# Kernel tuning notes

Measured on AMD Instinct MI355X. Metric: run time of the kernel, lower is better.

The kernel has to match this reference:

```python
import jax, jax.numpy as jnp
import numpy as np
import math

B, T, D, N = 4, 1024, 768, 7  # batch, seq, d_model, n_chambers
STEP, WARMUP = 4000, 2000      # curriculum: step past warmup -> all masks ~1
INIT_SCALE = 0.01


def _curriculum_masks():
    # NautilusScheduler.get_masks: smooth sigmoid activation per chamber (static floats)
    slope = 8.0 * N / WARMUP
    return [1.0 / (1.0 + math.exp(-slope * (STEP - WARMUP * (i + 0.5) / N))) for i in range(N)]


def _layernorm(x, g, b, eps=1e-5):
    m = jnp.mean(x, axis=-1, keepdims=True)
    v = jnp.mean((x - m) ** 2, axis=-1, keepdims=True)
    return (x - m) * jax.lax.rsqrt(v + eps) * g + b


def _chamber(h, Wq, Wk, gw, gb, sp, mask_val, causal):
    # get_bias stand-in: bilinear content bias (B,T,T)
    q = h @ Wq                                   # (B,T,D)
    k = h @ Wk                                   # (B,T,D)
    bias = jnp.einsum('btd,bsd->bts', q, k) / jnp.sqrt(jnp.asarray(D, h.dtype))
    bias = jnp.where(causal[None], bias, -jnp.inf)   # causal masked_fill
    w = jnp.nan_to_num(jax.nn.softmax(bias, axis=-1))
    enrichment = jnp.einsum('bts,bsd->btd', w, h) - h
    gate = jax.nn.sigmoid(h @ gw[:, None] + gb)      # (B,T,1)
    scale = jax.nn.softplus(sp)                      # learnable positive scale
    return scale * gate * mask_val * enrichment


def setup_inputs() -> dict:
    key = jax.random.key(0)
    ks = jax.random.split(key, 8)
    x = jax.random.normal(ks[0], (B, T, D), jnp.float32)
    s = 1.0 / np.sqrt(D)
    Wq = jax.random.normal(ks[1], (N, D, D), jnp.float32) * s
    Wk = jax.random.normal(ks[2], (N, D, D), jnp.float32) * s
    gate_w = jax.random.normal(ks[3], (N, D), jnp.float32) * 0.02
    gate_b = jnp.zeros((N,), jnp.float32)
    # per-chamber softplus-inverse init: log(exp(init*(1+3*prog))-1+1e-6)
    sp = np.array([math.log(math.exp(INIT_SCALE * (1.0 + 3.0 * i / (N - 1))) - 1.0 + 1e-6)
                   for i in range(N)], dtype=np.float32)
    scale_p = jnp.asarray(sp)
    merge_W = jax.random.normal(ks[4], (D, N * D), jnp.float32) * (1.0 / np.sqrt(N * D))
    return {
        'x': x, 'Wq': Wq, 'Wk': Wk, 'gate_w': gate_w, 'gate_b': gate_b,
        'scale_p': scale_p, 'merge_W': merge_W,
        'mode_logit': jnp.float32(0.0), 'residual_gate': jnp.float32(0.1),
        'ln_pre_g': jnp.ones((D,), jnp.float32), 'ln_pre_b': jnp.zeros((D,), jnp.float32),
        'ln_post_g': jnp.ones((D,), jnp.float32), 'ln_post_b': jnp.zeros((D,), jnp.float32),
    }


def reference(x, Wq, Wk, gate_w, gate_b, scale_p, merge_W, mode_logit,
              residual_gate, ln_pre_g, ln_pre_b, ln_post_g, ln_post_b):
    masks = _curriculum_masks()
    causal = jnp.tril(jnp.ones((T, T), bool))
    h = _layernorm(x, ln_pre_g, ln_pre_b)
    mode_gate = jax.nn.sigmoid(mode_logit)
    seq = jnp.zeros_like(h)
    deltas = []
    for i in range(N):  # fixed small structural loop over chambers
        seq = seq + _chamber(h + seq, Wq[i], Wk[i], gate_w[i], gate_b[i],
                             scale_p[i], masks[i], causal)
        deltas.append(_chamber(h, Wq[i], Wk[i], gate_w[i], gate_b[i],
                               scale_p[i], masks[i], causal))
    par = jnp.concatenate(deltas, axis=-1) @ merge_W.T  # (B,T,D)
    enrichment = (1.0 - mode_gate) * seq + mode_gate * par
    enrichment = _layernorm(enrichment, ln_post_g, ln_post_b)
    return x + residual_gate * enrichment
```

## Files before the change

kernel.cpp:

```cpp
#include <hip/hip_runtime.h>
#include <math.h>

#define D_MODEL 768
#define T_SEQ   1024
#define BATCH   4
#define NCH     7
#define ROWS    4096
#define KM      (NCH * D_MODEL)

typedef unsigned short u16;
typedef __attribute__((ext_vector_type(8))) short bh8;
typedef __attribute__((ext_vector_type(4))) float f32x4;

__device__ __forceinline__ u16 f2bf(float f) {
    union { float f; unsigned u; } v; v.f = f;
    return (u16)((v.u + 0x7fffu + ((v.u >> 16) & 1u)) >> 16);
}
__device__ __forceinline__ float bf2f(u16 b) {
    union { unsigned u; float f; } v; v.u = ((unsigned)b) << 16;
    return v.f;
}
__device__ __forceinline__ float wred_sum(float v) {
    #pragma unroll
    for (int o = 32; o; o >>= 1) v += __shfl_down(v, o, 64);
    return v;
}
__device__ __forceinline__ float wred_max(float v) {
    #pragma unroll
    for (int o = 32; o; o >>= 1) v = fmaxf(v, __shfl_down(v, o, 64));
    return v;
}
__device__ __forceinline__ float chamber_mask(int i) {
    float slope = 8.0f * 7.0f / 2000.0f;
    return 1.0f / (1.0f + __expf(-slope * (4000.0f - 2000.0f * (i + 0.5f) / 7.0f)));
}

#define GLD16(g, l) __builtin_amdgcn_global_load_lds( \
    (const __attribute__((address_space(1))) void*)(g), \
    (__attribute__((address_space(3))) void*)(l), 16, 0, 0)

__device__ __forceinline__ int xcd_swizzle(int gflat, int Ntot) {
    if ((Ntot & 7) == 0) {
        int chunk = Ntot >> 3;
        gflat = (gflat & 7) * chunk + (gflat >> 3);
    }
    return gflat;
}

__device__ __forceinline__ int slot_f(int row) { return (row >> 1) & 3; }

__global__ __launch_bounds__(256)
void gemm_nt_kernel(const u16* __restrict__ A, const u16* __restrict__ B,
                    void* __restrict__ Cv,
                    int K, int lda, int ldb, int ldc,
                    long long sA1, long long sA2, long long sB1, long long sB2,
                    long long sC1, long long sC2, int zm,
                    float alpha, int mode, int causal_skip, int causal_k,
                    int kss, int klen)
{
    int gx = gridDim.x, gy = gridDim.y;
    int Ntot = gx * gy * gridDim.z;
    int gflat = xcd_swizzle(blockIdx.x + gx * (blockIdx.y + gy * blockIdx.z), Ntot);
    int bn = gflat % gx;
    int rest = gflat / gx;
    int bm = rest % gy;
    int bz = rest / gy;
    if (causal_skip && bn > bm) return;
    int bz1 = bz % zm, bz2 = bz / zm;

    const u16* Ab = A + bz1 * sA1 + bz2 * sA2 + (long long)(bm * 128) * lda;
    const u16* Bb = B + bz1 * sB1 + bz2 * sB2 + (long long)(bn * 128) * ldb;

    __shared__ u16 sm[4 * 128 * 32];
    u16* Al0 = sm;
    u16* Bl0 = sm + 128 * 32;
    u16* Al1 = sm + 2 * 128 * 32;
    u16* Bl1 = sm + 3 * 128 * 32;

    int tid  = threadIdx.x;
    int lane = tid & 63;
    int wave = tid >> 6;
    int wm = wave >> 1, wn = wave & 1;

    int k_begin = kss ? bz1 * kss : 0;
    int k_end   = klen ? (k_begin + klen) : K;
    if (causal_k) k_end = min(k_end, (bm + 1) * 128);

    f32x4 acc[4][4];
    #pragma unroll
    for (int i = 0; i < 4; i++)
        #pragma unroll
        for (int j = 0; j < 4; j++)
            acc[i][j] = (f32x4){0.f, 0.f, 0.f, 0.f};

    int srow = lane >> 2;
    int skq  = (lane & 3) * 8;
    int fm   = lane & 15;
    int fk   = (lane >> 4) * 8;

    for (int k0 = k_begin; k0 < k_end; k0 += 64) {
        __syncthreads();
        #pragma unroll
        for (int r = 0; r < 2; r++) {
            int row = r * 64 + wave * 16 + srow;
            long long ra = (long long)row * lda + k0 + skq;
            long long rb2 = (long long)row * ldb + k0 + skq;
            GLD16(Ab + ra,       Al0 + row * 32 + skq);
            GLD16(Bb + rb2,      Bl0 + row * 32 + skq);
            GLD16(Ab + ra + 32,  Al1 + row * 32 + skq);
            GLD16(Bb + rb2 + 32, Bl1 + row * 32 + skq);
        }
        __syncthreads();

        #pragma unroll
        for (int p = 0; p < 2; p++) {
            const u16* Al = p ? Al1 : Al0;
            const u16* Bl = p ? Bl1 : Bl0;
            bh8 af[4], bf[4];
            #pragma unroll
            for (int i = 0; i < 4; i++)
                af[i] = *(const bh8*)(Al + (wm * 64 + i * 16 + fm) * 32 + fk);
            #pragma unroll
            for (int j = 0; j < 4; j++)
                bf[j] = *(const bh8*)(Bl + (wn * 64 + j * 16 + fm) * 32 + fk);
            #pragma unroll
            for (int i = 0; i < 4; i++)
                #pragma unroll
                for (int j = 0; j < 4; j++)
                    acc[i][j] = __builtin_amdgcn_mfma_f32_16x16x32_bf16(af[i], bf[j], acc[i][j], 0, 0, 0);
        }
    }

    int rbase = bm * 128 + wm * 64 + (lane >> 4) * 4;
    int cbase = bn * 128 + wn * 64 + (lane & 15);
    long long zoff = bz1 * sC1 + bz2 * sC2;
    if (mode == 1) {
        u16* C = (u16*)Cv + zoff;
        #pragma unroll
        for (int i = 0; i < 4; i++)
            #pragma unroll
            for (int j = 0; j < 4; j++)
                #pragma unroll
                for (int r = 0; r < 4; r++)
                    C[(long long)(rbase + i * 16 + r) * ldc + cbase + j * 16] = f2bf(acc[i][j][r] * alpha);
    } else if (mode == 3) {
        u16* C = (u16*)Cv + zoff;
        #pragma unroll
        for (int i = 0; i < 4; i++)
            #pragma unroll
            for (int j = 0; j < 4; j++)
                #pragma unroll
                for (int r = 0; r < 4; r++) {
                    union { _Float16 h; u16 u; } cv;
                    cv.h = (_Float16)(acc[i][j][r] * alpha);
                    C[(long long)(rbase + i * 16 + r) * ldc + cbase + j * 16] = cv.u;
                }
    } else {
        float* C = (float*)Cv + zoff;
        #pragma unroll
        for (int i = 0; i < 4; i++)
            #pragma unroll
            for (int j = 0; j < 4; j++)
                #pragma unroll
                for (int r = 0; r < 4; r++)
                    C[(long long)(rbase + i * 16 + r) * ldc + cbase + j * 16] = acc[i][j][r] * alpha;
    }
}

__global__ __launch_bounds__(256)
void gemm64_nt_kernel(const u16* __restrict__ A, const u16* __restrict__ B,
                      void* __restrict__ Cv,
                      int K, int lda, int ldb, int ldc,
                      long long sA1, long long sA2, long long sB1, long long sB2,
                      long long sC1, long long sC2, int zm,
                      float alpha, int mode, int causal_skip, int causal_k,
                      int tri, int lptrev,
                      float* __restrict__ hhfp, const float* __restrict__ coefp,
                      u16* __restrict__ hbsp, u16* __restrict__ htsp,
                      const float* __restrict__ hp, u16* __restrict__ dbp)
{
    int bn, bm, bz;
    if (tri) {
        int Ntot = gridDim.x;
        int f = xcd_swizzle(blockIdx.x, Ntot);
        bz = f / tri;
        int r = f - bz * tri;
        bm = (int)((sqrtf(8.0f * (float)r + 1.0f) - 1.0f) * 0.5f);
        while ((bm + 1) * (bm + 2) / 2 <= r) bm++;
        while (bm * (bm + 1) / 2 > r) bm--;
        bn = r - bm * (bm + 1) / 2;
    } else {
        int gx = gridDim.x, gy = gridDim.y;
        int Ntot = gx * gy * gridDim.z;
        int gflat = xcd_swizzle(blockIdx.x + gx * (blockIdx.y + gy * blockIdx.z), Ntot);
        bn = gflat % gx;
        int rest = gflat / gx;
        bm = rest % gy;
        bz = rest / gy;
        if (lptrev) bm = gy - 1 - bm;
        if (causal_skip && bn > bm) return;
    }
    int bz1 = bz % zm, bz2 = bz / zm;

    const u16* Ab = A + bz1 * sA1 + bz2 * sA2 + (long long)(bm * 64) * lda;
    const u16* Bb = B + bz1 * sB1 + bz2 * sB2 + (long long)(bn * 64) * ldb;

    __shared__ u16 sm[8 * 64 * 32];
    const int PS = 64 * 32;

    int tid  = threadIdx.x;
    int lane = tid & 63;
    int wave = tid >> 6;

    int k_end = causal_k ? min(K, (bm + 1) * 64) : K;

    f32x4 acc[4];
    #pragma unroll
    for (int j = 0; j < 4; j++) acc[j] = (f32x4){0.f, 0.f, 0.f, 0.f};

    int srow   = tid >> 2;
    int schunk = (tid & 3) * 8;
    int scq    = ((tid & 3) ^ slot_f(srow)) * 8;
    int fm     = lane & 15;
    int fk     = (lane >> 4) * 8;

    int k0 = 0;
    while (k0 < k_end) {
        __syncthreads();
        if (k_end - k0 >= 128) {
            #pragma unroll
            for (int p = 0; p < 4; p++) {
                long long ra  = (long long)srow * lda + k0 + p * 32 + scq;
                long long rb2 = (long long)srow * ldb + k0 + p * 32 + scq;
                GLD16(Ab + ra,  sm + (2 * p) * PS + srow * 32 + schunk);
                GLD16(Bb + rb2, sm + (2 * p + 1) * PS + srow * 32 + schunk);
            }
            __syncthreads();
            #pragma unroll
            for (int p = 0; p < 4; p++) {
                const u16* Al = sm + (2 * p) * PS;
                const u16* Bl = sm + (2 * p + 1) * PS;
                int Ra = wave * 16 + fm;
                bh8 af = *(const bh8*)(Al + Ra * 32 + (fk ^ (slot_f(Ra) * 8)));
                bh8 bf[4];
                #pragma unroll
                for (int j = 0; j < 4; j++) {
                    int Rb = j * 16 + fm;
                    bf[j] = *(const bh8*)(Bl + Rb * 32 + (fk ^ (slot_f(Rb) * 8)));
                }
                #pragma unroll
                for (int j = 0; j < 4; j++)
                    acc[j] = __builtin_amdgcn_mfma_f32_16x16x32_bf16(af, bf[j], acc[j], 0, 0, 0);
            }
            k0 += 128;
        } else {
            #pragma unroll
            for (int p = 0; p < 2; p++) {
                long long ra  = (long long)srow * lda + k0 + p * 32 + scq;
                long long rb2 = (long long)srow * ldb + k0 + p * 32 + scq;
                GLD16(Ab + ra,  sm + (2 * p) * PS + srow * 32 + schunk);
                GLD16(Bb + rb2, sm + (2 * p + 1) * PS + srow * 32 + schunk);
            }
            __syncthreads();
            #pragma unroll
            for (int p = 0; p < 2; p++) {
                const u16* Al = sm + (2 * p) * PS;
                const u16* Bl = sm + (2 * p + 1) * PS;
                int Ra = wave * 16 + fm;
                bh8 af = *(const bh8*)(Al + Ra * 32 + (fk ^ (slot_f(Ra) * 8)));
                bh8 bf[4];
                #pragma unroll
                for (int j = 0; j < 4; j++) {
                    int Rb = j * 16 + fm;
                    bf[j] = *(const bh8*)(Bl + Rb * 32 + (fk ^ (slot_f(Rb) * 8)));
                }
                #pragma unroll
                for (int j = 0; j < 4; j++)
                    acc[j] = __builtin_amdgcn_mfma_f32_16x16x32_bf16(af, bf[j], acc[j], 0, 0, 0);
            }
            k0 += 64;
        }
    }

    int rbase = bm * 64 + wave * 16 + (lane >> 4) * 4;
    int cbase = bn * 64 + (lane & 15);
    long long zoff = bz1 * sC1 + bz2 * sC2;
    if (mode == 1) {
        u16* C = (u16*)Cv + zoff;
        #pragma unroll
        for (int j = 0; j < 4; j++)
            #pragma unroll
            for (int r = 0; r < 4; r++)
                C[(long long)(rbase + r) * ldc + cbase + j * 16] = f2bf(acc[j][r] * alpha);
    } else if (mode == 3) {
        u16* C = (u16*)Cv + zoff;
        #pragma unroll
        for (int j = 0; j < 4; j++)
            #pragma unroll
            for (int r = 0; r < 4; r++) {
                union { _Float16 h; u16 u; } cv;
                cv.h = (_Float16)(acc[j][r] * alpha);
                C[(long long)(rbase + r) * ldc + cbase + j * 16] = cv.u;
            }
    } else if (mode == 5) {
        int b = bz1, ch = bz2;
        #pragma unroll
        for (int r = 0; r < 4; r++) {
            int t = rbase + r;
            long long rowg = (long long)b * T_SEQ + t;
            float cf = coefp[(long long)ch * ROWS + rowg];
            #pragma unroll
            for (int j = 0; j < 4; j++) {
                int d = cbase + j * 16;
                float hv = hp[rowg * D_MODEL + d];
                dbp[rowg * KM + ch * D_MODEL + d] = f2bf(cf * (acc[j][r] - hv));
            }
        }
    } else if (mode == 6) {
        __syncthreads();
        u16* tile = sm;
        #pragma unroll
        for (int r = 0; r < 4; r++) {
            int t = rbase + r;
            long long rowg = (long long)bz1 * T_SEQ + t;
            float cf = coefp[rowg];
            int tl = t - bm * 64;
            #pragma unroll
            for (int j = 0; j < 4; j++) {
                int d = cbase + j * 16;
                long long idx = rowg * D_MODEL + d;
                float v = hhfp[idx];
                float nh = v + cf * (acc[j][r] - v);
                hhfp[idx] = nh;
                u16 w = f2bf(nh);
                hbsp[idx] = w;
                tile[((lane & 15) + j * 16) * 66 + tl] = w;
            }
        }
        __syncthreads();
        int dl = tid >> 2, tch = (tid & 3) * 16;
        long long ob = (long long)bz1 * T_SEQ * D_MODEL +
                       (long long)(bn * 64 + dl) * T_SEQ + bm * 64 + tch;
        #pragma unroll
        for (int kk = 0; kk < 16; kk++)
            htsp[ob + kk] = tile[dl * 66 + tch + kk];
    } else {
        float* C = (float*)Cv + zoff;
        #pragma unroll
        for (int j = 0; j < 4; j++)
            #pragma unroll
            for (int r = 0; r < 4; r++)
                C[(long long)(rbase + r) * ldc + cbase + j * 16] = acc[j][r] * alpha;
    }
}

__global__ __launch_bounds__(256)
void ln_pre_kernel(const float* __restrict__ x, const float* __restrict__ g,
                   const float* __restrict__ b, float* __restrict__ h,
                   float* __restrict__ hhf, u16* __restrict__ hbp,
                   u16* __restrict__ hbs)
{
    int row = blockIdx.x;
    long long base = (long long)row * D_MODEL;
    int tid = threadIdx.x, lane = tid & 63, wave = tid >> 6;
    __shared__ float red[4];
    float v[3]; float s = 0.f;
    #pragma unroll
    for (int k = 0; k < 3; k++) { v[k] = x[base + tid + k * 256]; s += v[k]; }
    s = wred_sum(s);
    if (lane == 0) red[wave] = s;
    __syncthreads();
    float mean = (red[0] + red[1] + red[2] + red[3]) * (1.f / D_MODEL);
    __syncthreads();
    float sq = 0.f;
    #pragma unroll
    for (int k = 0; k < 3; k++) { float dd = v[k] - mean; sq += dd * dd; }
    sq = wred_sum(sq);
    if (lane == 0) red[wave] = sq;
    __syncthreads();
    float var = (red[0] + red[1] + red[2] + red[3]) * (1.f / D_MODEL);
    float rstd = rsqrtf(var + 1e-5f);
    #pragma unroll
    for (int k = 0; k < 3; k++) {
        int c = tid + k * 256;
        float o = (v[k] - mean) * rstd * g[c] + b[c];
        h[base + c] = o; hhf[base + c] = o;
        u16 w = f2bf(o);
        hbp[base + c] = w; hbs[base + c] = w;
    }
}

__global__ __launch_bounds__(256)
void transpose2_kernel(const u16* __restrict__ hb, u16* __restrict__ htp,
                       u16* __restrict__ hts)
{
    __shared__ u16 tile[32][33];
    int b = blockIdx.z;
    int d0 = blockIdx.x * 32, t0 = blockIdx.y * 32;
    int tx = threadIdx.x & 31, ty = threadIdx.x >> 5;
    long long bb = (long long)b * T_SEQ * D_MODEL;
    #pragma unroll
    for (int i = 0; i < 32; i += 8)
        tile[ty + i][tx] = hb[bb + (long long)(t0 + ty + i) * D_MODEL + d0 + tx];
    __syncthreads();
    #pragma unroll
    for (int i = 0; i < 32; i += 8) {
        long long o = bb + (long long)(d0 + ty + i) * T_SEQ + t0 + tx;
        u16 w = tile[tx][ty + i];
        htp[o] = w; hts[o] = w;
    }
}

__device__ __forceinline__ void softmax_row(u16* row, int len, int tid, int lane, int wave,
                                            float* red)
{
    float ev[4];
    float m = -3.0e38f;
    #pragma unroll
    for (int k = 0; k < 4; k++) {
        int s = tid + k * 256;
        if (s < len) {
            union { u16 u; _Float16 h; } cv; cv.u = row[s];
            ev[k] = (float)cv.h;
        } else ev[k] = -3.0e38f;
        m = fmaxf(m, ev[k]);
    }
    m = wred_max(m);
    if (lane == 0) red[wave] = m;
    __syncthreads();
    m = fmaxf(fmaxf(red[0], red[1]), fmaxf(red[2], red[3]));
    __syncthreads();
    float sum = 0.f;
    #pragma unroll
    for (int k = 0; k < 4; k++) {
        int s = tid + k * 256;
        float e = (s < len) ? __expf(ev[k] - m) : 0.f;
        ev[k] = e; sum += e;
    }
    sum = wred_sum(sum);
    if (lane == 0) red[wave] = sum;
    __syncthreads();
    sum = red[0] + red[1] + red[2] + red[3];
    float inv = 1.f / sum;
    #pragma unroll
    for (int k = 0; k < 4; k++)
        row[tid + k * 256] = f2bf(ev[k] * inv);
}

__global__ __launch_bounds__(256)
void softmax_kernel(u16* __restrict__ SP)
{
    int t = blockIdx.x, z = blockIdx.y;
    __shared__ float red[4];
    int tid = threadIdx.x, lane = tid & 63, wave = tid >> 6;
    softmax_row(SP + (long long)z * T_SEQ * T_SEQ + (long long)t * T_SEQ,
                t + 1, tid, lane, wave, red);
}

__global__ __launch_bounds__(256)
void softmax_coef_kernel(u16* __restrict__ SP, const float* __restrict__ hhf,
                         const float* __restrict__ gw, const float* __restrict__ gb,
                         const float* __restrict__ sp, int ci,
                         float* __restrict__ coefS)
{
    int t = blockIdx.x, z = blockIdx.y;
    int tid = threadIdx.x, lane = tid & 63, wave = tid >> 6;
    if (z == BATCH) {
        int row = t * 4 + wave;
        long long base = (long long)row * D_MODEL;
        const float* g = gw + ci * D_MODEL;
        float dot = 0.f;
        #pragma unroll
        for (int k = 0; k < 12; k++) dot += hhf[base + lane + 64 * k] * g[lane + 64 * k];
        dot = wred_sum(dot);
        if (lane == 0) {
            float gate = 1.f / (1.f + __expf(-(dot + gb[ci])));
            coefS[row] = log1pf(expf(sp[ci])) * chamber_mask(ci) * gate;
        }
        return;
    }
    __shared__ float red[4];
    softmax_row(SP + (long long)z * T_SEQ * T_SEQ + (long long)t * T_SEQ,
                t + 1, tid, lane, wave, red);
}

__global__ __launch_bounds__(256)
void coef_par_kernel(const float* __restrict__ h, const float* __restrict__ gw,
                     const float* __restrict__ gb, const float* __restrict__ sp,
                     float* __restrict__ coefP)
{
    int row = blockIdx.x * 4 + (threadIdx.x >> 6);
    int lane = threadIdx.x & 63;
    long long base = (long long)row * D_MODEL;
    float hv[12];
    #pragma unroll
    for (int k = 0; k < 12; k++) hv[k] = h[base + lane + 64 * k];
    for (int ci = 0; ci < NCH; ci++) {
        const float* g = gw + ci * D_MODEL;
        float dot = 0.f;
        #pragma unroll
        for (int k = 0; k < 12; k++) dot += hv[k] * g[lane + 64 * k];
        dot = wred_sum(dot);
        if (lane == 0) {
            float gate = 1.f / (1.f + __expf(-(dot + gb[ci])));
            coefP[ci * ROWS + row] = log1pf(expf(sp[ci])) * chamber_mask(ci) * gate;
        }
    }
}

__global__ __launch_bounds__(256)
void cast4_kernel(const float4* __restrict__ in, ushort4* __restrict__ outp, int n4)
{
    int i = blockIdx.x * 256 + threadIdx.x;
    if (i < n4) {
        float4 v = in[i];
        ushort4 o;
        o.x = f2bf(v.x); o.y = f2bf(v.y); o.z = f2bf(v.z); o.w = f2bf(v.w);
        outp[i] = o;
    }
}

__global__ __launch_bounds__(256)
void final_kernel(const float* __restrict__ x, const float* __restrict__ h,
                  const float* __restrict__ hhf, const u16* __restrict__ Pp,
                  const float* __restrict__ mode_logit, const float* __restrict__ residual_gate,
                  const float* __restrict__ g, const float* __restrict__ b,
                  float* __restrict__ out)
{
    const long long RDe = (long long)ROWS * D_MODEL;
    int row = blockIdx.x;
    long long base = (long long)row * D_MODEL;
    int tid = threadIdx.x, lane = tid & 63, wave = tid >> 6;
    __shared__ float red[4];
    float mg = 1.f / (1.f + __expf(-mode_logit[0]));
    float rg = residual_gate[0];
    float e[3]; float s = 0.f;
    #pragma unroll
    for (int k = 0; k < 3; k++) {
        int c = tid + k * 256;
        float p = 0.f;
        #pragma unroll
        for (int z = 0; z < NCH; z++) p += bf2f(Pp[z * RDe + base + c]);
        float v = (1.f - mg) * (hhf[base + c] - h[base + c]) + mg * p;
        e[k] = v; s += v;
    }
    s = wred_sum(s);
    if (lane == 0) red[wave] = s;
    __syncthreads();
    float mean = (red[0] + red[1] + red[2] + red[3]) * (1.f / D_MODEL);
    __syncthreads();
    float sq = 0.f;
    #pragma unroll
    for (int k = 0; k < 3; k++) { float dd = e[k] - mean; sq += dd * dd; }
    sq = wred_sum(sq);
    if (lane == 0) red[wave] = sq;
    __syncthreads();
    float var = (red[0] + red[1] + red[2] + red[3]) * (1.f / D_MODEL);
    float rstd = rsqrtf(var + 1e-5f);
    #pragma unroll
    for (int k = 0; k < 3; k++) {
        int c = tid + k * 256;
        out[base + c] = x[base + c] + rg * ((e[k] - mean) * rstd * g[c] + b[c]);
    }
}

extern "C" void kernel_launch(void* const* d_in, const int* in_sizes, int n_in,
                              void* d_out, int out_size, void* d_ws, size_t ws_size,
                              hipStream_t stream)
{
    (void)in_sizes; (void)n_in; (void)out_size; (void)ws_size;
    const float* x             = (const float*)d_in[0];
    const float* Wq            = (const float*)d_in[1];
    const float* Wk            = (const float*)d_in[2];
    const float* gate_w        = (const float*)d_in[3];
    const float* gate_b        = (const float*)d_in[4];
    const float* scale_p       = (const float*)d_in[5];
    const float* merge_W       = (const float*)d_in[6];
    const float* mode_logit    = (const float*)d_in[7];
    const float* residual_gate = (const float*)d_in[8];
    const float* ln_pre_g      = (const float*)d_in[9];
    const float* ln_pre_b      = (const float*)d_in[10];
    const float* ln_post_g     = (const float*)d_in[11];
    const float* ln_post_b     = (const float*)d_in[12];
    float* out = (float*)d_out;

    const long long DD  = (long long)D_MODEL * D_MODEL;
    const long long TD  = (long long)T_SEQ * D_MODEL;
    const long long TTs = (long long)T_SEQ * T_SEQ;
    const long long RDe = (long long)ROWS * D_MODEL;
    const int NTRI = 16 * 17 / 2;

    size_t off = 0;
    char* wsb = (char*)d_ws;
    auto alloc = [&](size_t bytes) -> void* {
        void* p = wsb + off; off += (bytes + 255) & ~(size_t)255; return p;
    };
    u16*   Mtb  = (u16*)alloc((size_t)NCH * DD * 2);
    u16*   mgb  = (u16*)alloc((size_t)D_MODEL * KM * 2);
    float* h    = (float*)alloc(RDe * 4);
    float* hhf  = (float*)alloc(RDe * 4);
    u16*   hbp  = (u16*)alloc(RDe * 2);
    u16*   htp  = (u16*)alloc(RDe * 2);
    u16*   hbs  = (u16*)alloc(RDe * 2);
    u16*   hts0 = (u16*)alloc(RDe * 2);
    u16*   hts1 = (u16*)alloc(RDe * 2);
    u16*   Spar = (u16*)alloc((size_t)(NCH * BATCH) * TTs * 2);
    u16*   Sseq = (u16*)alloc((size_t)BATCH * TTs * 2);
    u16*   Upar = (u16*)alloc((size_t)NCH * RDe * 2);
    u16*   Useq = (u16*)alloc(RDe * 2);
    u16*   db   = (u16*)alloc((size_t)ROWS * KM * 2);
    float* coefP= (float*)alloc((size_t)NCH * ROWS * 4);
    float* coefS= (float*)alloc((size_t)ROWS * 4);
    u16*   Wqb  = Spar;
    u16*   Wkb  = Spar + (size_t)NCH * DD;
    u16*   Pp   = Upar;

    const float sc = 1.0f / sqrtf((float)D_MODEL);
    const int N4W = (int)((size_t)NCH * DD) / 4;
    const int N4M = (int)((size_t)D_MODEL * KM) / 4;

    ln_pre_kernel<<<ROWS, 256, 0, stream>>>(x, ln_pre_g, ln_pre_b, h, hhf, hbp, hbs);
    cast4_kernel<<<(N4W + 255) / 256, 256, 0, stream>>>((const float4*)Wq, (ushort4*)Wqb, N4W);
    cast4_kernel<<<(N4W + 255) / 256, 256, 0, stream>>>((const float4*)Wk, (ushort4*)Wkb, N4W);
    cast4_kernel<<<(N4M + 255) / 256, 256, 0, stream>>>((const float4*)merge_W, (ushort4*)mgb, N4M);
    transpose2_kernel<<<dim3(24, 32, BATCH), 256, 0, stream>>>(hbp, htp, hts0);
    coef_par_kernel<<<ROWS / 4, 256, 0, stream>>>(h, gate_w, gate_b, scale_p, coefP);

    gemm_nt_kernel<<<dim3(6, 6, NCH), 256, 0, stream>>>(
        Wkb, Wqb, Mtb, D_MODEL, D_MODEL, D_MODEL, D_MODEL,
        DD, 0, DD, 0, DD, 0, NCH, 1.f, 1, 0, 0, 0, 0);

    gemm_nt_kernel<<<dim3(6, 32, NCH), 256, 0, stream>>>(
        hbp, Mtb, Upar, D_MODEL, D_MODEL, D_MODEL, D_MODEL,
        0, 0, DD, 0, RDe, 0, NCH, 1.f, 1, 0, 0, 0, 0);
    gemm64_nt_kernel<<<dim3(NTRI * BATCH * NCH), 256, 0, stream>>>(
        Upar, hbp, Spar, D_MODEL, D_MODEL, D_MODEL, T_SEQ,
        TD, RDe, TD, 0, TTs, 4 * TTs, BATCH, sc, 3, 0, 0, NTRI, 0,
        nullptr, nullptr, nullptr, nullptr, nullptr, nullptr);
    softmax_kernel<<<dim3(T_SEQ, BATCH * NCH), 256, 0, stream>>>(Spar);
    gemm64_nt_kernel<<<dim3(12, 16, BATCH * NCH), 256, 0, stream>>>(
        Spar, htp, nullptr, T_SEQ, T_SEQ, T_SEQ, D_MODEL,
        TTs, 4 * TTs, TD, 0, 0, 0, BATCH, 1.f, 5, 0, 1, 0, 1,
        nullptr, coefP, nullptr, nullptr, h, db);
    gemm_nt_kernel<<<dim3(6, 32, NCH), 256, 0, stream>>>(
        db, mgb, Pp, KM, KM, KM, D_MODEL,
        0, 0, 0, 0, RDe, 0, NCH, 1.f, 1, 0, 0, D_MODEL, D_MODEL);

    u16* htsCur = hts0;
    u16* htsNxt = hts1;
    for (int i = 0; i < NCH; i++) {
        gemm64_nt_kernel<<<dim3(12, 64, 1), 256, 0, stream>>>(
            hbs, Mtb + (long long)i * DD, Useq,
            D_MODEL, D_MODEL, D_MODEL, D_MODEL, 0, 0, 0, 0, 0, 0, 1,
            1.f, 1, 0, 0, 0, 0,
            nullptr, nullptr, nullptr, nullptr, nullptr, nullptr);
        gemm64_nt_kernel<<<dim3(NTRI * BATCH), 256, 0, stream>>>(
            Useq, hbs, Sseq, D_MODEL, D_MODEL, D_MODEL, T_SEQ,
            TD, 0, TD, 0, TTs, 0, BATCH, sc, 3, 0, 0, NTRI, 0,
            nullptr, nullptr, nullptr, nullptr, nullptr, nullptr);
        softmax_coef_kernel<<<dim3(T_SEQ, BATCH + 1), 256, 0, stream>>>(
            Sseq, hhf, gate_w, gate_b, scale_p, i, coefS);
        gemm64_nt_kernel<<<dim3(12, 16, BATCH), 256, 0, stream>>>(
            Sseq, htsCur, nullptr, T_SEQ, T_SEQ, T_SEQ, D_MODEL,
            TTs, 0, TD, 0, 0, 0, BATCH, 1.f, 6, 0, 1, 0, 1,
            hhf, coefS, hbs, htsNxt, nullptr, nullptr);
        u16* tmp = htsCur; htsCur = htsNxt; htsNxt = tmp;
    }

    final_kernel<<<ROWS, 256, 0, stream>>>(x, h, hhf, Pp, mode_logit, residual_gate,
                                           ln_post_g, ln_post_b, out);
}
```

Before: 768.3 us.

## Fuse causal softmax into PV GEMM via online softmax; fold gate coef into score GEMM

The standalone softmax kernels are removed. The PV GEMM (modes 5 and 6) now reads raw fp16 scores tile by tile and applies causal masking, a running max and sum, rescaling and bf16 probability conversion in registers before the MFMA. The per-chamber gate/scale coefficient is computed by extra blocks appended to the triangular score GEMM grid, so that work no longer needs its own launch. This removes a full read-modify-write pass over the T×T score matrices and several launches. In exchange the PV loop does exp and shuffle work on every 64-wide K tile and loses the 128-wide K unroll.

```diff
diff --git a/kernel.cpp b/kernel.cpp
--- a/kernel.cpp
+++ b/kernel.cpp
@@ -23,11 +23,6 @@
 __device__ __forceinline__ float wred_sum(float v) {
     #pragma unroll
     for (int o = 32; o; o >>= 1) v += __shfl_down(v, o, 64);
-    return v;
-}
-__device__ __forceinline__ float wred_max(float v) {
-    #pragma unroll
-    for (int o = 32; o; o >>= 1) v = fmaxf(v, __shfl_down(v, o, 64));
     return v;
 }
 __device__ __forceinline__ float chamber_mask(int i) {
@@ -174,15 +169,36 @@
                       long long sA1, long long sA2, long long sB1, long long sB2,
                       long long sC1, long long sC2, int zm,
                       float alpha, int mode, int causal_skip, int causal_k,
-                      int tri, int lptrev,
+                      int tri, int lptrev, int ntri_blk,
                       float* __restrict__ hhfp, const float* __restrict__ coefp,
                       u16* __restrict__ hbsp, u16* __restrict__ htsp,
                       const float* __restrict__ hp, u16* __restrict__ dbp)
 {
+    int tid  = threadIdx.x;
+    int lane = tid & 63;
+    int wave = tid >> 6;
+
     int bn, bm, bz;
     if (tri) {
         int Ntot = gridDim.x;
         int f = xcd_swizzle(blockIdx.x, Ntot);
+        if (ntri_blk && f >= ntri_blk) {
+            int rowg = (f - ntri_blk) * 4 + wave;
+            long long base = (long long)rowg * D_MODEL;
+            const float* gwp = (const float*)hbsp;
+            const float* gbp = (const float*)htsp;
+            int ci = lptrev;
+            float dot = 0.f;
+            #pragma unroll
+            for (int k = 0; k < 12; k++)
+                dot += coefp[base + lane + 64 * k] * gwp[ci * D_MODEL + lane + 64 * k];
+            dot = wred_sum(dot);
+            if (lane == 0) {
+                float gate = 1.f / (1.f + __expf(-(dot + gbp[ci])));
+                hhfp[rowg] = log1pf(expf(hp[ci])) * chamber_mask(ci) * gate;
+            }
+            return;
+        }
         bz = f / tri;
         int r = f - bz * tri;
         bm = (int)((sqrtf(8.0f * (float)r + 1.0f) - 1.0f) * 0.5f);
@@ -208,10 +224,6 @@
     __shared__ u16 sm[8 * 64 * 32];
     const int PS = 64 * 32;
 
-    int tid  = threadIdx.x;
-    int lane = tid & 63;
-    int wave = tid >> 6;
-
     int k_end = causal_k ? min(K, (bm + 1) * 64) : K;
 
     f32x4 acc[4];
@@ -224,24 +236,73 @@
     int fm     = lane & 15;
     int fk     = (lane >> 4) * 8;
 
-    int k0 = 0;
-    while (k0 < k_end) {
-        __syncthreads();
-        if (k_end - k0 >= 128) {
-            #pragma unroll
-            for (int p = 0; p < 4; p++) {
-                long long ra  = (long long)srow * lda + k0 + p * 32 + scq;
-                long long rb2 = (long long)srow * ldb + k0 + p * 32 + scq;
+    if (mode == 5 || mode == 6) {
+        float m_run = -3.0e38f, s_run = 0.f;
+        int row_l = wave * 16 + fm;
+        int nkt = k_end >> 6;
+        for (int kt = 0; kt < nkt; kt++) {
+            int k0b = kt << 6;
+            __syncthreads();
+            #pragma unroll
+            for (int p = 0; p < 2; p++) {
+                long long ra  = (long long)srow * lda + k0b + p * 32 + scq;
+                long long rb2 = (long long)srow * ldb + k0b + p * 32 + scq;
                 GLD16(Ab + ra,  sm + (2 * p) * PS + srow * 32 + schunk);
                 GLD16(Bb + rb2, sm + (2 * p + 1) * PS + srow * 32 + schunk);
             }
             __syncthreads();
-            #pragma unroll
-            for (int p = 0; p < 4; p++) {
-                const u16* Al = sm + (2 * p) * PS;
+            int aoff = fk ^ (slot_f(row_l) * 8);
+            bh8 a0 = *(const bh8*)(sm + 0 * PS + row_l * 32 + aoff);
+            bh8 a1 = *(const bh8*)(sm + 2 * PS + row_l * 32 + aoff);
+            float v[16];
+            #pragma unroll
+            for (int e = 0; e < 8; e++) {
+                union { u16 u; _Float16 h; } c0, c1;
+                c0.u = (u16)a0[e]; c1.u = (u16)a1[e];
+                v[e] = (float)c0.h; v[8 + e] = (float)c1.h;
+            }
+            if (kt == nkt - 1) {
+                #pragma unroll
+                for (int e = 0; e < 8; e++) {
+                    if (fk + e > row_l)      v[e]     = -3.0e38f;
+                    if (32 + fk + e > row_l) v[8 + e] = -3.0e38f;
+                }
+            }
+            float tmax = v[0];
+            #pragma unroll
+            for (int e = 1; e < 16; e++) tmax = fmaxf(tmax, v[e]);
+            tmax = fmaxf(tmax, __shfl_xor(tmax, 16, 64));
+            tmax = fmaxf(tmax, __shfl_xor(tmax, 32, 64));
+            float m_new = fmaxf(m_run, tmax);
+            float scale = __expf(m_run - m_new);
+            float psum = 0.f;
+            u16 pb[16];
+            #pragma unroll
+            for (int e = 0; e < 16; e++) {
+                float pe = __expf(v[e] - m_new);
+                psum += pe;
+                pb[e] = f2bf(pe);
+            }
+            psum += __shfl_xor(psum, 16, 64);
+            psum += __shfl_xor(psum, 32, 64);
+            s_run = s_run * scale + psum;
+            m_run = m_new;
+            float fr[4];
+            #pragma unroll
+            for (int r = 0; r < 4; r++)
+                fr[r] = __shfl(scale, ((lane >> 4) << 2) + r, 64);
+            #pragma unroll
+            for (int j = 0; j < 4; j++)
+                #pragma unroll
+                for (int r = 0; r < 4; r++)
+                    acc[j][r] *= fr[r];
+            bh8 pa0, pa1;
+            #pragma unroll
+            for (int e = 0; e < 8; e++) { pa0[e] = (short)pb[e]; pa1[e] = (short)pb[8 + e]; }
+            #pragma unroll
+            for (int p = 0; p < 2; p++) {
                 const u16* Bl = sm + (2 * p + 1) * PS;
-                int Ra = wave * 16 + fm;
-                bh8 af = *(const bh8*)(Al + Ra * 32 + (fk ^ (slot_f(Ra) * 8)));
+                bh8 pa = p ? pa1 : pa0;
                 bh8 bf[4];
                 #pragma unroll
                 for (int j = 0; j < 4; j++) {
@@ -250,35 +311,75 @@
                 }
                 #pragma unroll
                 for (int j = 0; j < 4; j++)
-                    acc[j] = __builtin_amdgcn_mfma_f32_16x16x32_bf16(af, bf[j], acc[j], 0, 0, 0);
-            }
-            k0 += 128;
-        } else {
-            #pragma unroll
-            for (int p = 0; p < 2; p++) {
-                long long ra  = (long long)srow * lda + k0 + p * 32 + scq;
-                long long rb2 = (long long)srow * ldb + k0 + p * 32 + scq;
-                GLD16(Ab + ra,  sm + (2 * p) * PS + srow * 32 + schunk);
-                GLD16(Bb + rb2, sm + (2 * p + 1) * PS + srow * 32 + schunk);
-            }
+                    acc[j] = __builtin_amdgcn_mfma_f32_16x16x32_bf16(pa, bf[j], acc[j], 0, 0, 0);
+            }
+        }
+        float invs[4];
+        #pragma unroll
+        for (int r = 0; r < 4; r++)
+            invs[r] = 1.f / __shfl(s_run, ((lane >> 4) << 2) + r, 64);
+        #pragma unroll
+        for (int j = 0; j < 4; j++)
+            #pragma unroll
+            for (int r = 0; r < 4; r++)
+                acc[j][r] *= invs[r];
+    } else {
+        int k0 = 0;
+        while (k0 < k_end) {
             __syncthreads();
-            #pragma unroll
-            for (int p = 0; p < 2; p++) {
-                const u16* Al = sm + (2 * p) * PS;
-                const u16* Bl = sm + (2 * p + 1) * PS;
-                int Ra = wave * 16 + fm;
-                bh8 af = *(const bh8*)(Al + Ra * 32 + (fk ^ (slot_f(Ra) * 8)));
-                bh8 bf[4];
-                #pragma unroll
-                for (int j = 0; j < 4; j++) {
-                    int Rb = j * 16 + fm;
-                    bf[j] = *(const bh8*)(Bl + Rb * 32 + (fk ^ (slot_f(Rb) * 8)));
+            if (k_end - k0 >= 128) {
+                #pragma unroll
+                for (int p = 0; p < 4; p++) {
+                    long long ra  = (long long)srow * lda + k0 + p * 32 + scq;
+                    long long rb2 = (long long)srow * ldb + k0 + p * 32 + scq;
+                    GLD16(Ab + ra,  sm + (2 * p) * PS + srow * 32 + schunk);
+                    GLD16(Bb + rb2, sm + (2 * p + 1) * PS + srow * 32 + schunk);
                 }
-                #pragma unroll
-                for (int j = 0; j < 4; j++)
-                    acc[j] = __builtin_amdgcn_mfma_f32_16x16x32_bf16(af, bf[j], acc[j], 0, 0, 0);
-            }
-            k0 += 64;
+                __syncthreads();
+                #pragma unroll
+                for (int p = 0; p < 4; p++) {
+                    const u16* Al = sm + (2 * p) * PS;
+                    const u16* Bl = sm + (2 * p + 1) * PS;
+                    int Ra = wave * 16 + fm;
+                    bh8 af = *(const bh8*)(Al + Ra * 32 + (fk ^ (slot_f(Ra) * 8)));
+                    bh8 bf[4];
+                    #pragma unroll
+                    for (int j = 0; j < 4; j++) {
+                        int Rb = j * 16 + fm;
+                        bf[j] = *(const bh8*)(Bl + Rb * 32 + (fk ^ (slot_f(Rb) * 8)));
+                    }
+                    #pragma unroll
+                    for (int j = 0; j < 4; j++)
+                        acc[j] = __builtin_amdgcn_mfma_f32_16x16x32_bf16(af, bf[j], acc[j], 0, 0, 0);
+                }
+                k0 += 128;
+            } else {
+                #pragma unroll
+                for (int p = 0; p < 2; p++) {
+                    long long ra  = (long long)srow * lda + k0 + p * 32 + scq;
+                    long long rb2 = (long long)srow * ldb + k0 + p * 32 + scq;
+                    GLD16(Ab + ra,  sm + (2 * p) * PS + srow * 32 + schunk);
+                    GLD16(Bb + rb2, sm + (2 * p + 1) * PS + srow * 32 + schunk);
+                }
+                __syncthreads();
+                #pragma unroll
+                for (int p = 0; p < 2; p++) {
+                    const u16* Al = sm + (2 * p) * PS;
+                    const u16* Bl = sm + (2 * p + 1) * PS;
+                    int Ra = wave * 16 + fm;
+                    bh8 af = *(const bh8*)(Al + Ra * 32 + (fk ^ (slot_f(Ra) * 8)));
+                    bh8 bf[4];
+                    #pragma unroll
+                    for (int j = 0; j < 4; j++) {
+                        int Rb = j * 16 + fm;
+                        bf[j] = *(const bh8*)(Bl + Rb * 32 + (fk ^ (slot_f(Rb) * 8)));
+                    }
+                    #pragma unroll
+                    for (int j = 0; j < 4; j++)
+                        acc[j] = __builtin_amdgcn_mfma_f32_16x16x32_bf16(af, bf[j], acc[j], 0, 0, 0);
+                }
+                k0 += 64;
+            }
         }
     }
 
@@ -409,79 +510,6 @@
         u16 w = tile[tx][ty + i];
         htp[o] = w; hts[o] = w;
     }
-}
-
-__device__ __forceinline__ void softmax_row(u16* row, int len, int tid, int lane, int wave,
-                                            float* red)
-{
-    float ev[4];
-    float m = -3.0e38f;
-    #pragma unroll
-    for (int k = 0; k < 4; k++) {
-        int s = tid + k * 256;
-        if (s < len) {
-            union { u16 u; _Float16 h; } cv; cv.u = row[s];
-            ev[k] = (float)cv.h;
-        } else ev[k] = -3.0e38f;
-        m = fmaxf(m, ev[k]);
-    }
-    m = wred_max(m);
-    if (lane == 0) red[wave] = m;
-    __syncthreads();
-    m = fmaxf(fmaxf(red[0], red[1]), fmaxf(red[2], red[3]));
-    __syncthreads();
-    float sum = 0.f;
-    #pragma unroll
-    for (int k = 0; k < 4; k++) {
-        int s = tid + k * 256;
-        float e = (s < len) ? __expf(ev[k] - m) : 0.f;
-        ev[k] = e; sum += e;
-    }
-    sum = wred_sum(sum);
-    if (lane == 0) red[wave] = sum;
-    __syncthreads();
-    sum = red[0] + red[1] + red[2] + red[3];
-    float inv = 1.f / sum;
-    #pragma unroll
-    for (int k = 0; k < 4; k++)
-        row[tid + k * 256] = f2bf(ev[k] * inv);
-}
-
-__global__ __launch_bounds__(256)
-void softmax_kernel(u16* __restrict__ SP)
-{
-    int t = blockIdx.x, z = blockIdx.y;
-    __shared__ float red[4];
-    int tid = threadIdx.x, lane = tid & 63, wave = tid >> 6;
-    softmax_row(SP + (long long)z * T_SEQ * T_SEQ + (long long)t * T_SEQ,
-                t + 1, tid, lane, wave, red);
-}
-
-__global__ __launch_bounds__(256)
-void softmax_coef_kernel(u16* __restrict__ SP, const float* __restrict__ hhf,
-                         const float* __restrict__ gw, const float* __restrict__ gb,
-                         const float* __restrict__ sp, int ci,
-                         float* __restrict__ coefS)
-{
-    int t = blockIdx.x, z = blockIdx.y;
-    int tid = threadIdx.x, lane = tid & 63, wave = tid >> 6;
-    if (z == BATCH) {
-        int row = t * 4 + wave;
-        long long base = (long long)row * D_MODEL;
-        const float* g = gw + ci * D_MODEL;
-        float dot = 0.f;
-        #pragma unroll
-        for (int k = 0; k < 12; k++) dot += hhf[base + lane + 64 * k] * g[lane + 64 * k];
-        dot = wred_sum(dot);
-        if (lane == 0) {
-            float gate = 1.f / (1.f + __expf(-(dot + gb[ci])));
-            coefS[row] = log1pf(expf(sp[ci])) * chamber_mask(ci) * gate;
-        }
-        return;
-    }
-    __shared__ float red[4];
-    softmax_row(SP + (long long)z * T_SEQ * T_SEQ + (long long)t * T_SEQ,
-                t + 1, tid, lane, wave, red);
 }
 
 __global__ __launch_bounds__(256)
@@ -635,12 +663,11 @@
         0, 0, DD, 0, RDe, 0, NCH, 1.f, 1, 0, 0, 0, 0);
     gemm64_nt_kernel<<<dim3(NTRI * BATCH * NCH), 256, 0, stream>>>(
         Upar, hbp, Spar, D_MODEL, D_MODEL, D_MODEL, T_SEQ,
-        TD, RDe, TD, 0, TTs, 4 * TTs, BATCH, sc, 3, 0, 0, NTRI, 0,
+        TD, RDe, TD, 0, TTs, 4 * TTs, BATCH, sc, 3, 0, 0, NTRI, 0, 0,
         nullptr, nullptr, nullptr, nullptr, nullptr, nullptr);
-    softmax_kernel<<<dim3(T_SEQ, BATCH * NCH), 256, 0, stream>>>(Spar);
     gemm64_nt_kernel<<<dim3(12, 16, BATCH * NCH), 256, 0, stream>>>(
         Spar, htp, nullptr, T_SEQ, T_SEQ, T_SEQ, D_MODEL,
-        TTs, 4 * TTs, TD, 0, 0, 0, BATCH, 1.f, 5, 0, 1, 0, 1,
+        TTs, 4 * TTs, TD, 0, 0, 0, BATCH, 1.f, 5, 0, 1, 0, 1, 0,
         nullptr, coefP, nullptr, nullptr, h, db);
     gemm_nt_kernel<<<dim3(6, 32, NCH), 256, 0, stream>>>(
         db, mgb, Pp, KM, KM, KM, D_MODEL,
@@ -652,17 +679,17 @@
         gemm64_nt_kernel<<<dim3(12, 64, 1), 256, 0, stream>>>(
             hbs, Mtb + (long long)i * DD, Useq,
             D_MODEL, D_MODEL, D_MODEL, D_MODEL, 0, 0, 0, 0, 0, 0, 1,
-            1.f, 1, 0, 0, 0, 0,
+            1.f, 1, 0, 0, 0, 0, 0,
             nullptr, nullptr, nullptr, nullptr, nullptr, nullptr);
-        gemm64_nt_kernel<<<dim3(NTRI * BATCH), 256, 0, stream>>>(
+        gemm64_nt_kernel<<<dim3(NTRI * BATCH + ROWS / 4), 256, 0, stream>>>(
             Useq, hbs, Sseq, D_MODEL, D_MODEL, D_MODEL, T_SEQ,
-            TD, 0, TD, 0, TTs, 0, BATCH, sc, 3, 0, 0, NTRI, 0,
-            nullptr, nullptr, nullptr, nullptr, nullptr, nullptr);
-        softmax_coef_kernel<<<dim3(T_SEQ, BATCH + 1), 256, 0, stream>>>(
-            Sseq, hhf, gate_w, gate_b, scale_p, i, coefS);
+            TD, 0, TD, 0, TTs, 0, BATCH, sc, 3, 0, 0, NTRI,  i,
+             NTRI * BATCH,
+             coefS,  hhf, (u16*)gate_w, (u16*)gate_b,
+            scale_p, nullptr);
         gemm64_nt_kernel<<<dim3(12, 16, BATCH), 256, 0, stream>>>(
             Sseq, htsCur, nullptr, T_SEQ, T_SEQ, T_SEQ, D_MODEL,
-            TTs, 0, TD, 0, 0, 0, BATCH, 1.f, 6, 0, 1, 0, 1,
+            TTs, 0, TD, 0, 0, 0, BATCH, 1.f, 6, 0, 1, 0, 1, 0,
             hhf, coefS, hbs, htsNxt, nullptr, nullptr);
         u16* tmp = htsCur; htsCur = htsNxt; htsNxt = tmp;
     }
```

Result: slower. 867.4 us (+12.9%).
